# Kernel tuning notes

Hardware: AMD Instinct MI355X
Metric: run time of the kernel (lower is better)

Reference implementation:

```python
import jax, jax.numpy as jnp
import numpy as np

B = 64
E = 512          # latent_size / h_dim
H = 8            # num_heads
D = E // H       # head_dim
MAX_AGENTS = 254 # max(agents_per_sample) for the deterministic counts below
NEG = -1e9


def setup_inputs() -> dict:
    key = jax.random.key(0)
    k_x, k_wi, k_bi, k_wo, k_bo = jax.random.split(key, 5)
    # deterministic variable agent counts in [128, 254]; sum == 11531, max == 254
    agents = jnp.array([128 + (3 * i) % 129 for i in range(B)], dtype=jnp.int32)
    total = 11531
    att_in = jax.random.normal(k_x, (total, E), dtype=jnp.float32)
    # nn.MultiheadAttention params: packed in-proj [3E, E] + bias, out-proj [E, E] + bias
    w_in = jax.random.normal(k_wi, (3 * E, E), dtype=jnp.float32) * 0.02
    b_in = jax.random.normal(k_bi, (3 * E,), dtype=jnp.float32) * 0.02
    w_out = jax.random.normal(k_wo, (E, E), dtype=jnp.float32) * 0.02
    b_out = jax.random.normal(k_bo, (E,), dtype=jnp.float32) * 0.02
    return {"att_in": att_in, "w_in": w_in, "b_in": b_in,
            "w_out": w_out, "b_out": b_out, "agents_per_sample": agents}


def reference(att_in, w_in, b_in, w_out, b_out, agents_per_sample):
    S = MAX_AGENTS
    # scatter packed rows into padded [B, S, E] via a clipped gather (jit-safe)
    offsets = jnp.cumsum(agents_per_sample) - agents_per_sample      # [B]
    pos = jnp.arange(S, dtype=jnp.int32)
    mask = pos[None, :] < agents_per_sample[:, None]                 # [B, S] valid
    idx = jnp.clip(offsets[:, None] + pos[None, :], 0, att_in.shape[0] - 1)
    padded = jnp.where(mask[..., None], att_in[idx], 0.0)            # [B, S, E]

    # fused QKV projection (torch packed in_proj), dropout disabled (eval)
    qkv = padded @ w_in.T + b_in                                     # [B, S, 3E]
    q, k, v = jnp.split(qkv, 3, axis=-1)
    q = q.reshape(B, S, H, D)
    k = k.reshape(B, S, H, D)
    v = v.reshape(B, S, H, D)

    scores = jnp.einsum('bqhd,bkhd->bhqk', q, k) * (D ** -0.5)      # [B, H, S, S]
    scores = jnp.where(mask[:, None, None, :], scores, NEG)          # key_padding_mask
    attn = jax.nn.softmax(scores, axis=-1)
    ctx = jnp.einsum('bhqk,bkhd->bqhd', attn, v).reshape(B, S, E)
    out = ctx @ w_out.T + b_out                                      # [B, S, E]
    # torch returns only valid rows per sample; zero the padded rows instead
    return out * mask[..., None]
```

## Files before the change

### kernel.cpp

```cpp
#include <hip/hip_runtime.h>
#include <hip/hip_bf16.h>

typedef __attribute__((ext_vector_type(8))) short bf16x8;
typedef __attribute__((ext_vector_type(4))) float f32x4;
typedef __attribute__((ext_vector_type(4))) int i32x4;
typedef __attribute__((ext_vector_type(4))) unsigned short u16x4;
typedef __attribute__((ext_vector_type(2))) unsigned ui2;
typedef __attribute__((ext_vector_type(4))) float fl4;

struct __attribute__((packed)) u16x4u { u16x4 v; };

__device__ __forceinline__ f32x4 mfma16(bf16x8 a, bf16x8 b, f32x4 c) {
    return __builtin_amdgcn_mfma_f32_16x16x32_bf16(a, b, c, 0, 0, 0);
}

__device__ __forceinline__ unsigned short f2b(float f) {
    unsigned u = __float_as_uint(f);
    unsigned r = (u + 0x7FFF + ((u >> 16) & 1)) >> 16;
    return (unsigned short)r;
}

__device__ __forceinline__ int bsearch_off(const int* s_off, int m) {
    int lo = 0, hi = 63;
    while (lo < hi) {
        int mid = (lo + hi + 1) >> 1;
        if (s_off[mid] <= m) lo = mid; else hi = mid - 1;
    }
    return lo;
}

__device__ __forceinline__ void gld_lds16(const __hip_bfloat16* g, __hip_bfloat16* l) {
    __builtin_amdgcn_global_load_lds(
        (const __attribute__((address_space(1))) void*)g,
        (__attribute__((address_space(3))) void*)l,
        16, 0, 0);
}

__global__ void k_prep(const unsigned short* __restrict__ src,
                       const void* __restrict__ b_in, const void* __restrict__ b_out,
                       const int* __restrict__ agents,
                       int* __restrict__ flag, int* __restrict__ offs,
                       float* __restrict__ bfi, float* __restrict__ bfo) {
    __shared__ int sh[256];
    __shared__ int sa[64];
    __shared__ int sflag;
    int tid = threadIdx.x;
    int h = 0;
    for (int i = tid; i < 16384; i += 256) {
        unsigned e = (src[i] >> 7) & 0xFF;
        if (e == 0xFF) h = 1;
    }
    sh[tid] = h;
    if (tid < 64) sa[tid] = agents[tid];
    __syncthreads();
    if (tid == 0) {
        int any = 0;
        for (int i = 0; i < 256; ++i) any |= sh[i];
        flag[0] = any;
        sflag = any;
    }
    if (tid < 64) {
        int ex = 0;
        for (int i = 0; i < 64; ++i) { int v = sa[i]; if (i < tid) ex += v; }
        offs[tid] = ex;
        if (tid == 63) offs[64] = ex + sa[63];
    }
    __syncthreads();
    int f = sflag;
    for (int i = tid; i < 1536; i += 256)
        bfi[i] = f ? ((const float*)b_in)[i]
                   : __bfloat162float(((const __hip_bfloat16*)b_in)[i]);
    for (int i = tid; i < 512; i += 256)
        bfo[i] = f ? ((const float*)b_out)[i]
                   : __bfloat162float(((const __hip_bfloat16*)b_out)[i]);
}

__global__ void k_zero_pad(char* __restrict__ out, const int* __restrict__ agents,
                           const int* __restrict__ flag) {
    int b = blockIdx.x;
    int n = agents[b];
    int esz = flag[0] ? 4 : 2;
    long long base = ((long long)b * 254 + n) * 512 * esz;
    long long bytes = (long long)(254 - n) * 512 * esz;
    for (long long i = ((long long)blockIdx.y * 256 + threadIdx.x) * 16;
         i < bytes; i += (long long)8 * 256 * 16)
        *(i32x4*)(out + base + i) = (i32x4){0, 0, 0, 0};
}

__global__ void k_cast_all(const void* __restrict__ sA, unsigned short* __restrict__ dA, int nA,
                           const void* __restrict__ sWi, unsigned short* __restrict__ dWi, int nWi,
                           const void* __restrict__ sWo, unsigned short* __restrict__ dWo, int nWo,
                           const int* __restrict__ flag) {
    int i = (blockIdx.x * 256 + threadIdx.x) * 4;
    const void* src; unsigned short* dst; int k;
    if (i < nA)            { src = sA;  dst = dA;  k = i; }
    else if (i < nA + nWi) { src = sWi; dst = dWi; k = i - nA; }
    else if (i < nA + nWi + nWo) { src = sWo; dst = dWo; k = i - nA - nWi; }
    else return;
    u16x4 o;
    if (flag[0]) {
        fl4 v = *(const fl4*)((const float*)src + k);
        o[0] = f2b(v[0]); o[1] = f2b(v[1]); o[2] = f2b(v[2]); o[3] = f2b(v[3]);
    } else {
        o = *(const u16x4*)((const unsigned short*)src + k);
    }
    *(u16x4*)(dst + k) = o;
}

template<int LDA, bool MROWS>
__device__ __forceinline__ void gemm_core(
    const __hip_bfloat16* __restrict__ A,
    const __hip_bfloat16* __restrict__ W,
    int m0, int n0, int total,
    __hip_bfloat16* As, __hip_bfloat16* Ws,
    f32x4 acc[4][4], int tid)
{
    int lane = tid & 63, quad = lane >> 4, c = lane & 15;
    int wave = tid >> 6;
    int wr = wave >> 1, wc = wave & 1;

    const __hip_bfloat16* gA[4];
    const __hip_bfloat16* gW[4];
    __hip_bfloat16* lA[4];
    __hip_bfloat16* lW[4];
#pragma unroll
    for (int j = 0; j < 4; ++j) {
        int L = j * 256 + tid;
        int row = L >> 3;
        int gseg = (L & 7) ^ (row & 7);
        int ar = m0 + row; if (ar > total - 1) ar = total - 1;
        gA[j] = A + (size_t)ar * LDA + gseg * 8;
        gW[j] = W + (size_t)(n0 + row) * 512 + gseg * 8;
        lA[j] = As + (size_t)(j * 256 + wave * 64) * 8;
        lW[j] = Ws + (size_t)(j * 256 + wave * 64) * 8;
    }

    for (int k0 = 0; k0 < 512; k0 += 64) {
        if (k0) __syncthreads();
#pragma unroll
        for (int j = 0; j < 4; ++j) gld_lds16(gA[j] + k0, lA[j]);
#pragma unroll
        for (int j = 0; j < 4; ++j) gld_lds16(gW[j] + k0, lW[j]);
        __syncthreads();
#pragma unroll
        for (int h = 0; h < 2; ++h) {
            bf16x8 af[4], wf[4];
#pragma unroll
            for (int t = 0; t < 4; ++t) {
                int rowa = wr * 64 + t * 16 + c;
                int rowb = wc * 64 + t * 16 + c;
                int ks = quad + 4 * h;
                af[t] = *(const bf16x8*)(As + (size_t)rowa * 64 + ((ks ^ (rowa & 7)) * 8));
                wf[t] = *(const bf16x8*)(Ws + (size_t)rowb * 64 + ((ks ^ (rowb & 7)) * 8));
            }
#pragma unroll
            for (int i = 0; i < 4; ++i)
#pragma unroll
                for (int j = 0; j < 4; ++j)
                    acc[i][j] = MROWS ? mfma16(af[i], wf[j], acc[i][j])
                                      : mfma16(wf[j], af[i], acc[i][j]);
        }
    }
}

__global__ __launch_bounds__(256) void k_qkv(
    const __hip_bfloat16* __restrict__ A,
    const __hip_bfloat16* __restrict__ W,
    const float* __restrict__ bias,
    const int* __restrict__ offs,
    __hip_bfloat16* __restrict__ qk,
    __hip_bfloat16* __restrict__ vT,
    int total, int MT)
{
    __shared__ __hip_bfloat16 As[128 * 64];
    __shared__ __hip_bfloat16 Ws[128 * 64];
    __shared__ int s_off[65];
    int l = blockIdx.x;
    int inner = l >> 3;
    int cb = inner % 12;
    int rb = (l & 7) + 8 * (inner / 12);
    if (rb >= MT) return;
    int n0 = cb * 128;
    int m0 = rb * 128;
    int tid = threadIdx.x;
    if (tid < 65) s_off[tid] = offs[tid];
    int lane = tid & 63, quad = lane >> 4, c = lane & 15;
    int wave = tid >> 6, wr = wave >> 1, wc = wave & 1;
    f32x4 z = {0.f, 0.f, 0.f, 0.f};
    f32x4 acc[4][4] = {{z,z,z,z},{z,z,z,z},{z,z,z,z},{z,z,z,z}};

    if (n0 < 1024) {
        gemm_core<512, false>(A, W, m0, n0, total, As, Ws, acc, tid);
        fl4 bv4[4];
#pragma unroll
        for (int j = 0; j < 4; ++j)
            bv4[j] = *(const fl4*)&bias[n0 + wc * 64 + j * 16 + quad * 4];
#pragma unroll
        for (int i = 0; i < 4; ++i) {
            int m = m0 + wr * 64 + i * 16 + c;
            if (m >= total) continue;
            size_t row = (size_t)m * 1024;
#pragma unroll
            for (int j = 0; j < 4; ++j) {
                int col0 = n0 + wc * 64 + j * 16 + quad * 4;
                u16x4 o;
#pragma unroll
                for (int r = 0; r < 4; ++r) o[r] = f2b(acc[i][j][r] + bv4[j][r]);
                *(u16x4*)&qk[row + col0] = o;
            }
        }
    } else {
        gemm_core<512, true>(A, W, m0, n0, total, As, Ws, acc, tid);
        float bv[4];
#pragma unroll
        for (int j = 0; j < 4; ++j) bv[j] = bias[n0 + wc * 64 + j * 16 + c];
#pragma unroll
        for (int i = 0; i < 4; ++i) {
            int m_base = m0 + wr * 64 + i * 16 + quad * 4;
            if (m_base >= total) continue;
            int lo = bsearch_off(s_off, m_base);
            bool vec = (m_base + 3 < total) && (s_off[lo + 1] > m_base + 3);
            if (vec) {
                int vs = m_base - s_off[lo];
#pragma unroll
                for (int j = 0; j < 4; ++j) {
                    int vc = n0 - 1024 + wc * 64 + j * 16 + c;
                    size_t idx = ((size_t)(lo * 8 + (vc >> 6)) * 64 + (vc & 63)) * 256 + vs;
                    u16x4 o;
#pragma unroll
                    for (int r = 0; r < 4; ++r) o[r] = f2b(acc[i][j][r] + bv[j]);
                    ((u16x4u*)&vT[idx])->v = o;
                }
            } else {
#pragma unroll
                for (int r = 0; r < 4; ++r) {
                    int m = m_base + r;
                    if (m >= total) continue;
                    int lo2 = bsearch_off(s_off, m);
                    int vs2 = m - s_off[lo2];
#pragma unroll
                    for (int j = 0; j < 4; ++j) {
                        int vc = n0 - 1024 + wc * 64 + j * 16 + c;
                        vT[((size_t)(lo2 * 8 + (vc >> 6)) * 64 + (vc & 63)) * 256 + vs2] =
                            __float2bfloat16(acc[i][j][r] + bv[j]);
                    }
                }
            }
        }
    }
}

__global__ __launch_bounds__(256, 2) void k_attn(
    __hip_bfloat16* __restrict__ qk,
    const __hip_bfloat16* __restrict__ vT,
    const int* __restrict__ agents,
    const int* __restrict__ offs)
{
    __shared__ __attribute__((aligned(16))) char Pl[4][16 * 80];
    int bh = blockIdx.x;
    int b = bh >> 3, h = bh & 7;
    int n = agents[b];
    int off = offs[b];
    int qtiles = (n + 15) >> 4;
    int stmax = (qtiles + 1) >> 1;
    int tid = threadIdx.x;
    int wave = tid >> 6, lane = tid & 63, quad = lane >> 4, c = lane & 15;
    const __hip_bfloat16* vbase = vT + (size_t)bh * 64 * 256;
    char* Plw = &Pl[wave][0];

    bf16x8 qB[4][2];
    int nt = 0;
#pragma unroll
    for (int t = 0; t < 4; ++t) {
        int qt = wave + 4 * t;
        if (qt < qtiles) {
            nt = t + 1;
            int qr = qt * 16 + c; if (qr > n - 1) qr = n - 1;
            const __hip_bfloat16* qp = qk + (size_t)(off + qr) * 1024 + h * 64 + quad * 8;
            qB[t][0] = *(const bf16x8*)qp;
            qB[t][1] = *(const bf16x8*)(qp + 32);
        }
    }

    f32x4 z = {0.f, 0.f, 0.f, 0.f};
    f32x4 O[4][4] = {{z,z,z,z},{z,z,z,z},{z,z,z,z},{z,z,z,z}};
    float sm[4] = {0.f, 0.f, 0.f, 0.f};
    const __hip_bfloat16* kg = qk + (size_t)off * 1024 + 512 + h * 64 + quad * 8;

    for (int st = 0; st < stmax; ++st) {
        int k0 = st * 32;
        bf16x8 kA[2][2];
#pragma unroll
        for (int ti = 0; ti < 2; ++ti) {
            int kr = k0 + ti * 16 + c; if (kr > n - 1) kr = n - 1;
            const __hip_bfloat16* kp = kg + (size_t)kr * 1024;
            kA[ti][0] = *(const bf16x8*)kp;
            kA[ti][1] = *(const bf16x8*)(kp + 32);
        }
        bf16x8 vA[4];
#pragma unroll
        for (int dt = 0; dt < 4; ++dt)
            vA[dt] = *(const bf16x8*)(vbase + (size_t)(dt * 16 + c) * 256 + k0 + quad * 8);

#pragma unroll
        for (int t = 0; t < 4; ++t) {
            if (t < nt) {
#pragma unroll
                for (int ti = 0; ti < 2; ++ti) {
                    f32x4 s = mfma16(kA[ti][0], qB[t][0], z);
                    s = mfma16(kA[ti][1], qB[t][1], s);
                    int kbase = k0 + ti * 16 + quad * 4;
                    float p0 = (kbase + 0 < n) ? __expf(s[0] * 0.125f) : 0.f;
                    float p1 = (kbase + 1 < n) ? __expf(s[1] * 0.125f) : 0.f;
                    float p2 = (kbase + 2 < n) ? __expf(s[2] * 0.125f) : 0.f;
                    float p3 = (kbase + 3 < n) ? __expf(s[3] * 0.125f) : 0.f;
                    sm[t] += (p0 + p1) + (p2 + p3);
                    ui2 dw;
                    dw[0] = (unsigned)f2b(p0) | ((unsigned)f2b(p1) << 16);
                    dw[1] = (unsigned)f2b(p2) | ((unsigned)f2b(p3) << 16);
                    *(ui2*)(Plw + c * 80 + ti * 32 + quad * 8) = dw;
                }
                bf16x8 pB = *(const bf16x8*)(Plw + c * 80 + quad * 16);
#pragma unroll
                for (int dt = 0; dt < 4; ++dt)
                    O[t][dt] = mfma16(vA[dt], pB, O[t][dt]);
            }
        }
    }

#pragma unroll
    for (int t = 0; t < 4; ++t) {
        if (t < nt) {
            float v = sm[t];
            v += __shfl_xor(v, 16);
            v += __shfl_xor(v, 32);
            float iv = 1.0f / v;
            int q = (wave + 4 * t) * 16 + c;
            if (q < n) {
                size_t row = (size_t)(off + q) * 1024 + h * 64;
#pragma unroll
                for (int dt = 0; dt < 4; ++dt) {
                    u16x4 o;
#pragma unroll
                    for (int r = 0; r < 4; ++r) o[r] = f2b(O[t][dt][r] * iv);
                    *(u16x4*)&qk[row + dt * 16 + quad * 4] = o;
                }
            }
        }
    }
}

__global__ __launch_bounds__(256) void k_out(
    const __hip_bfloat16* __restrict__ A,
    const __hip_bfloat16* __restrict__ W,
    const float* __restrict__ bias,
    const int* __restrict__ offs,
    void* __restrict__ out,
    const int* __restrict__ flag,
    int total, int MT)
{
    __shared__ __hip_bfloat16 As[128 * 64];
    __shared__ __hip_bfloat16 Ws[128 * 64];
    __shared__ int s_off[65];
    int l = blockIdx.x;
    int inner = l >> 3;
    int cb = inner & 3;
    int rb = (l & 7) + 8 * (inner >> 2);
    if (rb >= MT) return;
    int n0 = cb * 128;
    int m0 = rb * 128;
    int tid = threadIdx.x;
    if (tid < 65) s_off[tid] = offs[tid];
    f32x4 z = {0.f, 0.f, 0.f, 0.f};
    f32x4 acc[4][4] = {{z,z,z,z},{z,z,z,z},{z,z,z,z},{z,z,z,z}};
    gemm_core<1024, false>(A, W, m0, n0, total, As, Ws, acc, tid);

    int f32m = flag[0];
    int lane = tid & 63, quad = lane >> 4, c = lane & 15;
    int wave = tid >> 6, wr = wave >> 1, wc = wave & 1;
    fl4 bv4[4];
#pragma unroll
    for (int j = 0; j < 4; ++j)
        bv4[j] = *(const fl4*)&bias[n0 + wc * 64 + j * 16 + quad * 4];
#pragma unroll
    for (int i = 0; i < 4; ++i) {
        int m = m0 + wr * 64 + i * 16 + c;
        if (m >= total) continue;
        int lo = bsearch_off(s_off, m);
        int os_ = m - s_off[lo];
        size_t rowb = ((size_t)(lo * 254 + os_)) * 512;
#pragma unroll
        for (int j = 0; j < 4; ++j) {
            int col0 = n0 + wc * 64 + j * 16 + quad * 4;
            if (f32m) {
                fl4 o;
#pragma unroll
                for (int r = 0; r < 4; ++r) o[r] = acc[i][j][r] + bv4[j][r];
                *(fl4*)&((float*)out)[rowb + col0] = o;
            } else {
                u16x4 o;
#pragma unroll
                for (int r = 0; r < 4; ++r) o[r] = f2b(acc[i][j][r] + bv4[j][r]);
                *(u16x4*)&((__hip_bfloat16*)out)[rowb + col0] = o;
            }
        }
    }
}

extern "C" void kernel_launch(void* const* d_in, const int* in_sizes, int n_in,
                              void* d_out, int out_size, void* d_ws, size_t ws_size,
                              hipStream_t stream) {
    const void* att_in = d_in[0];
    const void* w_in   = d_in[1];
    const void* b_in   = d_in[2];
    const void* w_out  = d_in[3];
    const void* b_out  = d_in[4];
    const int* agents  = (const int*)d_in[5];
    int total = in_sizes[0] / 512;

    char* p = (char*)d_ws;
    int* flag  = (int*)p;                 p += 256;
    int* offs  = (int*)p;                 p += 512;
    float* bfi = (float*)p;               p += 1536 * 4;
    float* bfo = (float*)p;               p += 512 * 4;
    __hip_bfloat16* WinBf  = (__hip_bfloat16*)p;  p += (size_t)1536 * 512 * 2;
    __hip_bfloat16* WoutBf = (__hip_bfloat16*)p;  p += (size_t)512 * 512 * 2;
    __hip_bfloat16* Abf    = (__hip_bfloat16*)p;  p += (size_t)total * 512 * 2;
    __hip_bfloat16* qk     = (__hip_bfloat16*)p;  p += (size_t)total * 1024 * 2;
    __hip_bfloat16* vT     = (__hip_bfloat16*)p;  p += (size_t)64 * 8 * 64 * 256 * 2;

    int nA = total * 512, nWi = 1536 * 512, nWo = 512 * 512;
    int ntot = nA + nWi + nWo;

    k_prep<<<1, 256, 0, stream>>>((const unsigned short*)att_in, b_in, b_out,
                                  agents, flag, offs, bfi, bfo);
    k_zero_pad<<<dim3(64, 8), 256, 0, stream>>>((char*)d_out, agents, flag);
    k_cast_all<<<(ntot / 4 + 255) / 256, 256, 0, stream>>>(
        att_in, (unsigned short*)Abf, nA,
        w_in,   (unsigned short*)WinBf, nWi,
        w_out,  (unsigned short*)WoutBf, nWo, flag);

    int MT = (total + 127) / 128;
    int MTpad = ((MT + 7) / 8) * 8;
    k_qkv<<<12 * MTpad, 256, 0, stream>>>(Abf, WinBf, bfi, offs, qk, vT, total, MT);
    k_attn<<<512, 256, 0, stream>>>(qk, vT, agents, offs);
    k_out<<<4 * MTpad, 256, 0, stream>>>(qk, WoutBf, bfo, offs, d_out, flag, total, MT);
}
```

Measured before the change: 179.4 us.

## Double-buffer LDS tiles in the GEMM core to overlap loads with MFMA

The GEMM main loop now keeps two LDS buffers for the A and W tiles. It issues the global-to-LDS loads for the next K slice before running the MFMAs on the current slice, with one barrier per iteration instead of two. The goal is to hide global memory latency behind matrix math in both the QKV and output projection kernels. In exchange, the LDS footprint per block doubles, which can cut the number of resident blocks per CU.

Result: slower. 183.3 us (+2.2%).

```diff
diff --git a/kernel.cpp b/kernel.cpp
--- a/kernel.cpp
+++ b/kernel.cpp
@@ -135,13 +135,25 @@
         lW[j] = Ws + (size_t)(j * 256 + wave * 64) * 8;
     }
 
-    for (int k0 = 0; k0 < 512; k0 += 64) {
-        if (k0) __syncthreads();
-#pragma unroll
-        for (int j = 0; j < 4; ++j) gld_lds16(gA[j] + k0, lA[j]);
-#pragma unroll
-        for (int j = 0; j < 4; ++j) gld_lds16(gW[j] + k0, lW[j]);
-        __syncthreads();
+#pragma unroll
+    for (int j = 0; j < 4; ++j) gld_lds16(gA[j], lA[j]);
+#pragma unroll
+    for (int j = 0; j < 4; ++j) gld_lds16(gW[j], lW[j]);
+    __syncthreads();
+
+#pragma unroll
+    for (int s = 0; s < 8; ++s) {
+        const int cur = s & 1;
+        const int nxt = cur ^ 1;
+        if (s < 7) {
+            int k0 = (s + 1) * 64;
+#pragma unroll
+            for (int j = 0; j < 4; ++j) gld_lds16(gA[j] + k0, lA[j] + nxt * (128 * 64));
+#pragma unroll
+            for (int j = 0; j < 4; ++j) gld_lds16(gW[j] + k0, lW[j] + nxt * (128 * 64));
+        }
+        const __hip_bfloat16* Ab = As + cur * (128 * 64);
+        const __hip_bfloat16* Wb = Ws + cur * (128 * 64);
 #pragma unroll
         for (int h = 0; h < 2; ++h) {
             bf16x8 af[4], wf[4];
@@ -150,8 +162,8 @@
                 int rowa = wr * 64 + t * 16 + c;
                 int rowb = wc * 64 + t * 16 + c;
                 int ks = quad + 4 * h;
-                af[t] = *(const bf16x8*)(As + (size_t)rowa * 64 + ((ks ^ (rowa & 7)) * 8));
-                wf[t] = *(const bf16x8*)(Ws + (size_t)rowb * 64 + ((ks ^ (rowb & 7)) * 8));
+                af[t] = *(const bf16x8*)(Ab + (size_t)rowa * 64 + ((ks ^ (rowa & 7)) * 8));
+                wf[t] = *(const bf16x8*)(Wb + (size_t)rowb * 64 + ((ks ^ (rowb & 7)) * 8));
             }
 #pragma unroll
             for (int i = 0; i < 4; ++i)
@@ -160,6 +172,7 @@
                     acc[i][j] = MROWS ? mfma16(af[i], wf[j], acc[i][j])
                                       : mfma16(wf[j], af[i], acc[i][j]);
         }
+        if (s < 7) __syncthreads();
     }
 }
 
@@ -172,8 +185,8 @@
     __hip_bfloat16* __restrict__ vT,
     int total, int MT)
 {
-    __shared__ __hip_bfloat16 As[128 * 64];
-    __shared__ __hip_bfloat16 Ws[128 * 64];
+    __shared__ __hip_bfloat16 As[2 * 128 * 64];
+    __shared__ __hip_bfloat16 Ws[2 * 128 * 64];
     __shared__ int s_off[65];
     int l = blockIdx.x;
     int inner = l >> 3;
@@ -359,8 +372,8 @@
     const int* __restrict__ flag,
     int total, int MT)
 {
-    __shared__ __hip_bfloat16 As[128 * 64];
-    __shared__ __hip_bfloat16 Ws[128 * 64];
+    __shared__ __hip_bfloat16 As[2 * 128 * 64];
+    __shared__ __hip_bfloat16 Ws[2 * 128 * 64];
     __shared__ int s_off[65];
     int l = blockIdx.x;
     int inner = l >> 3;
```
